# Optimization experiments

Hardware: AMD Instinct MI355X
Metric: run time of the kernel (lower is better)

The kernel has to match this reference:

```python
import jax, jax.numpy as jnp
import numpy as np

B, C, H, W = 8, 256, 64, 64
K = 3                      # kernel size
DG = 4                     # deformable groups
PAD = (K - 1) // 2
K2 = K * K
GN_GROUPS = 32
EPS = 1e-5


def setup_inputs() -> dict:
    key = jax.random.key(0)
    ks = jax.random.split(key, 6)
    x = jax.random.normal(ks[0], (B, C, H, W), dtype=jnp.float32)
    shape = jax.random.normal(ks[1], (B, 4, H, W), dtype=jnp.float32)
    # 1x1 offset conv weight [dg*k*k*2, 4] (bias=False); small std keeps offsets sane
    w_offset = jax.random.normal(ks[2], (DG * K2 * 2, 4), dtype=jnp.float32) * 0.1
    # deformable conv weight [out_c, in_c, K, K]
    w_deform = jax.random.normal(ks[3], (C, C, K, K), dtype=jnp.float32) * 0.01
    gamma = jnp.ones((C,), dtype=jnp.float32)
    beta = jnp.zeros((C,), dtype=jnp.float32)
    return {"x": x, "shape": shape, "w_offset": w_offset,
            "w_deform": w_deform, "gamma": gamma, "beta": beta}


def _bilinear_sample(img, py, px):
    # img: [Cg, H, W]; py, px: [K2, H, W] absolute sampling coords
    h, w = img.shape[1], img.shape[2]
    y0 = jnp.floor(py)
    x0 = jnp.floor(px)
    ly = py - y0
    lx = px - x0

    def gather(yi, xi):
        valid = ((yi >= 0) & (yi <= h - 1) & (xi >= 0) & (xi <= w - 1)).astype(img.dtype)
        yc = jnp.clip(yi, 0, h - 1).astype(jnp.int32)
        xc = jnp.clip(xi, 0, w - 1).astype(jnp.int32)
        return img[:, yc, xc] * valid  # [Cg, K2, H, W]

    v00 = gather(y0, x0)
    v01 = gather(y0, x0 + 1)
    v10 = gather(y0 + 1, x0)
    v11 = gather(y0 + 1, x0 + 1)
    return (v00 * (1 - ly) * (1 - lx) + v01 * (1 - ly) * lx
            + v10 * ly * (1 - lx) + v11 * ly * lx)


def _forward(x, shape, w_offset, w_deform, gamma, beta):
    # offset = 1x1 conv on shape (detached in torch): [B, DG*K2*2, H, W]
    offset = jnp.einsum('oc,bchw->bohw', w_offset, shape)
    # mmcv layout: per group, per kernel position, (dy, dx)
    off = offset.reshape(B, DG, K2, 2, H, W)
    dy, dx = off[:, :, :, 0], off[:, :, :, 1]  # [B, DG, K2, H, W]

    ki = (jnp.arange(K2) // K - PAD).astype(jnp.float32)  # kernel row offsets
    kj = (jnp.arange(K2) % K - PAD).astype(jnp.float32)
    ys = jnp.arange(H, dtype=jnp.float32)
    xs = jnp.arange(W, dtype=jnp.float32)
    # absolute sampling positions [B, DG, K2, H, W]
    py = dy + ki[None, None, :, None, None] + ys[None, None, None, :, None]
    px = dx + kj[None, None, :, None, None] + xs[None, None, None, None, :]

    cg = C // DG
    x_g = x.reshape(B, DG, cg, H, W)
    # sampled: [B, DG, Cg, K2, H, W]
    sampled = jax.vmap(jax.vmap(_bilinear_sample))(x_g, py, px)

    w = w_deform.reshape(C, DG, cg, K2)
    out = jnp.einsum('bgckhw,ogck->bohw', sampled, w)  # [B, C, H, W]

    # GroupNorm(32, C) + ReLU
    og = out.reshape(B, GN_GROUPS, C // GN_GROUPS, H, W)
    mu = og.mean(axis=(2, 3, 4), keepdims=True)
    var = og.var(axis=(2, 3, 4), keepdims=True)
    norm = ((og - mu) * jax.lax.rsqrt(var + EPS)).reshape(B, C, H, W)
    y = norm * gamma[None, :, None, None] + beta[None, :, None, None]
    return jax.nn.relu(y)


def reference(x, shape, w_offset, w_deform, gamma, beta):
    return _forward(x, shape, w_offset, w_deform, gamma, beta)
```

## Files before the change

kernel.cpp:

```cpp
#include <hip/hip_runtime.h>
#include <hip/hip_bf16.h>

#define EPSV 1e-5f

typedef __attribute__((ext_vector_type(8))) short short8;
typedef __attribute__((ext_vector_type(4))) float f32x4;
typedef __attribute__((ext_vector_type(2))) float f32x2;
typedef __attribute__((ext_vector_type(4))) unsigned u32x4;

#define W2_BYTES 1179648ull

__global__ __launch_bounds__(256) void wt2_kernel(const float* __restrict__ wd,
                                                  __hip_bfloat16* __restrict__ w2,
                                                  float* __restrict__ st) {
  int idx = blockIdx.x * 256 + threadIdx.x;
  int c  = idx & 31;
  int r  = idx >> 5;
  int k  = r % 9;
  int r2 = r / 9;
  int p  = r2 & 7;
  int o  = r2 >> 3;
  w2[idx] = __float2bfloat16(wd[(o * 256 + p * 32 + c) * 9 + k]);
  if (blockIdx.x < 2) st[blockIdx.x * 256 + threadIdx.x] = 0.f;
}

static __device__ __forceinline__ f32x2 unpk(unsigned u) {
  union { unsigned i; float f; } lo, hi;
  lo.i = u << 16;
  hi.i = u & 0xffff0000u;
  return (f32x2){lo.f, hi.f};
}

static __device__ __forceinline__ unsigned pkbf(float a, float b) {
  __hip_bfloat162 p = __float22bfloat162_rn(make_float2(a, b));
  return *(unsigned*)&p;
}

__global__ __launch_bounds__(512, 2) void fused_kernel(
    const float* __restrict__ x, const float* __restrict__ shp,
    const float* __restrict__ woff, const __hip_bfloat16* __restrict__ w2,
    float* __restrict__ out, float* __restrict__ st) {
  __shared__ __align__(16) unsigned short sX[2][8 * 64 * 32];
  __shared__ __align__(16) unsigned short sB[2][128 * 32];
  __shared__ float sW[288];

  const int b    = blockIdx.x & 7;
  const int band = blockIdx.x >> 3;
  const int h0   = band << 1;
  const int t    = threadIdx.x;
  const int wv   = t >> 6, lane = t & 63;
  const int quad = lane >> 4, l15 = lane & 15;

  const float* xb = x + ((size_t)b << 20);
  const unsigned short* w2b = (const unsigned short*)w2;

  if (t < 288) sW[t] = woff[t];

  if (wv < 4) {
    const int cw = wv;
    const unsigned short* aro =
        w2b + (size_t)((cw << 6) + l15) * 2304 + (quad << 3);

    f32x4 acc[4][8];
#pragma unroll
    for (int mo = 0; mo < 4; ++mo)
#pragma unroll
      for (int np = 0; np < 8; ++np) acc[mo][np] = (f32x4){0.f, 0.f, 0.f, 0.f};

    short8 afc[4];
#pragma unroll
    for (int mo = 0; mo < 4; ++mo)
      afc[mo] = *(const short8*)(aro + (size_t)(mo << 4) * 2304);

    asm volatile("s_waitcnt lgkmcnt(0)" ::: "memory");
    asm volatile("s_barrier" ::: "memory");
    asm volatile("s_barrier" ::: "memory");

    for (int it = 0; it < 72; ++it) {
      const unsigned short* Bc = sB[it & 1];
#pragma unroll
      for (int np = 0; np < 8; ++np) {
        const int row = (np << 4) + l15;
        short8 bf = *(const short8*)&Bc[(row << 5) + ((quad ^ ((row >> 1) & 3)) << 3)];
#pragma unroll
        for (int mo = 0; mo < 4; ++mo)
          acc[mo][np] = __builtin_amdgcn_mfma_f32_16x16x32_bf16(afc[mo], bf, acc[mo][np], 0, 0, 0);
      }
      if (it < 71) {
#pragma unroll
        for (int mo = 0; mo < 4; ++mo)
          afc[mo] = *(const short8*)(aro + (size_t)(mo << 4) * 2304 + (size_t)((it + 1) << 5));
      }
      asm volatile("s_barrier" ::: "memory");
    }

#pragma unroll
    for (int mo = 0; mo < 4; ++mo) {
      float s = 0.f, q = 0.f;
#pragma unroll
      for (int np = 0; np < 8; ++np)
#pragma unroll
        for (int r = 0; r < 4; ++r) { float v = acc[mo][np][r]; s += v; q += v * v; }
#pragma unroll
      for (int m = 1; m < 16; m <<= 1) { s += __shfl_xor(s, m, 64); q += __shfl_xor(q, m, 64); }
      if (l15 == 0) {
        int gid = (b << 5) + (cw << 3) + (mo << 1) + (quad >> 1);
        atomicAdd(&st[gid], s);
        atomicAdd(&st[256 + gid], q);
      }
    }

    float* ob = out + (((size_t)((b << 8) + (cw << 6))) << 12) + (band << 7);
#pragma unroll
    for (int mo = 0; mo < 4; ++mo)
#pragma unroll
      for (int np = 0; np < 8; ++np)
#pragma unroll
        for (int r = 0; r < 4; ++r)
          ob[((size_t)((mo << 4) + (quad << 2) + r) << 12) + (np << 4) + l15] = acc[mo][np][r];
  } else {
    const int pid   = t - 256;
    const int n     = pid & 127;
    const int chalf = pid >> 7;
    const int pxl   = n & 63;
    const int h     = h0 + (n >> 6);
    const int spx   = pid & 63;
    const int sc8   = (pid >> 6) & 3;
    const int wslot = (sc8 ^ ((spx >> 1) & 3)) << 3;

    float a0 = shp[((size_t)(b * 4 + 0) << 12) + (h << 6) + pxl];
    float a1 = shp[((size_t)(b * 4 + 1) << 12) + (h << 6) + pxl];
    float a2 = shp[((size_t)(b * 4 + 2) << 12) + (h << 6) + pxl];
    float a3 = shp[((size_t)(b * 4 + 3) << 12) + (h << 6) + pxl];

    {
      const float* xph = xb + ((size_t)(sc8 << 3) << 12) + spx;
#pragma unroll
      for (int j = 0; j < 8; ++j) {
        const int grow = min(max(h0 - 3 + j, 0), 63);
        float v[8];
#pragma unroll
        for (int jj = 0; jj < 8; ++jj) v[jj] = xph[(jj << 12) + (grow << 6)];
        *(u32x4*)&sX[0][(((j << 6) + spx) << 5) + wslot] =
            (u32x4){pkbf(v[0], v[1]), pkbf(v[2], v[3]), pkbf(v[4], v[5]), pkbf(v[6], v[7])};
      }
    }

    auto produce = [&](int tp, int tk, int buf) {
      const float* wp = &sW[(((tp >> 1) * 9 + tk)) << 3];
      float dy = wp[0]*a0 + wp[1]*a1 + wp[2]*a2 + wp[3]*a3;
      float dx = wp[4]*a0 + wp[5]*a1 + wp[6]*a2 + wp[7]*a3;
      float py  = dy + (float)(h + tk / 3 - 1);
      float pxp = dx + (float)(pxl + tk % 3 - 1);
      float y0f = floorf(py), x0f = floorf(pxp);
      float ly = py - y0f, lx = pxp - x0f;
      int y0 = (int)y0f, x0 = (int)x0f;
      float m_y0 = (y0 >=  0 && y0 <= 63) ? 1.f : 0.f;
      float m_y1 = (y0 >= -1 && y0 <= 62) ? 1.f : 0.f;
      float m_x0 = (x0 >=  0 && x0 <= 63) ? 1.f : 0.f;
      float m_x1 = (x0 >= -1 && x0 <= 62) ? 1.f : 0.f;
      float w00 = (1.f - ly) * (1.f - lx) * m_y0 * m_x0;
      float w01 = (1.f - ly) * lx         * m_y0 * m_x1;
      float w10 = ly         * (1.f - lx) * m_y1 * m_x0;
      float w11 = ly         * lx         * m_y1 * m_x1;
      int yc0 = min(max(y0, 0), 63),     yc1 = min(max(y0 + 1, 0), 63);
      int xc0 = min(max(x0, 0), 63),     xc1 = min(max(x0 + 1, 0), 63);
      int ry0 = min(max(yc0 - (h0 - 3), 0), 7);
      int ry1 = min(max(yc1 - (h0 - 3), 0), 7);
      const unsigned short* Xc = sX[tp & 1];
      const int s0 = chalf << 1;
      const int z0 = (xc0 >> 1) & 3, z1 = (xc1 >> 1) & 3;
      const int ba = ((ry0 << 6) + xc0) << 5, bb2 = ((ry0 << 6) + xc1) << 5;
      const int bc = ((ry1 << 6) + xc0) << 5, bd = ((ry1 << 6) + xc1) << 5;
      uint4 A0 = *(const uint4*)&Xc[ba  + ((s0 ^ z0) << 3)];
      uint4 A1 = *(const uint4*)&Xc[ba  + (((s0 + 1) ^ z0) << 3)];
      uint4 B0 = *(const uint4*)&Xc[bb2 + ((s0 ^ z1) << 3)];
      uint4 B1 = *(const uint4*)&Xc[bb2 + (((s0 + 1) ^ z1) << 3)];
      uint4 C0 = *(const uint4*)&Xc[bc  + ((s0 ^ z0) << 3)];
      uint4 C1 = *(const uint4*)&Xc[bc  + (((s0 + 1) ^ z0) << 3)];
      uint4 D0 = *(const uint4*)&Xc[bd  + ((s0 ^ z1) << 3)];
      uint4 D1 = *(const uint4*)&Xc[bd  + (((s0 + 1) ^ z1) << 3)];
      unsigned ua[8] = {A0.x, A0.y, A0.z, A0.w, A1.x, A1.y, A1.z, A1.w};
      unsigned ub[8] = {B0.x, B0.y, B0.z, B0.w, B1.x, B1.y, B1.z, B1.w};
      unsigned uc[8] = {C0.x, C0.y, C0.z, C0.w, C1.x, C1.y, C1.z, C1.w};
      unsigned ud[8] = {D0.x, D0.y, D0.z, D0.w, D1.x, D1.y, D1.z, D1.w};
      unsigned ov[8];
#pragma unroll
      for (int j = 0; j < 8; ++j) {
        f32x2 v = unpk(ua[j]) * w00 + unpk(ub[j]) * w01
                + unpk(uc[j]) * w10 + unpk(ud[j]) * w11;
        ov[j] = pkbf(v.x, v.y);
      }
      const int nb5 = n << 5;
      const int zn = (n >> 1) & 3;
      *(u32x4*)&sB[buf][nb5 + ((s0 ^ zn) << 3)]       = (u32x4){ov[0], ov[1], ov[2], ov[3]};
      *(u32x4*)&sB[buf][nb5 + (((s0 + 1) ^ zn) << 3)] = (u32x4){ov[4], ov[5], ov[6], ov[7]};
    };

    auto commit8 = [&](const float* v, int row, int nb) {
      *(u32x4*)&sX[nb][(((row << 6) + spx) << 5) + wslot] =
          (u32x4){pkbf(v[0], v[1]), pkbf(v[2], v[3]), pkbf(v[4], v[5]), pkbf(v[6], v[7])};
    };

    asm volatile("s_waitcnt lgkmcnt(0)" ::: "memory");
    asm volatile("s_barrier" ::: "memory");

    produce(0, 0, 0);
    asm volatile("s_waitcnt lgkmcnt(0)" ::: "memory");
    asm volatile("s_barrier" ::: "memory");

    float xrA[8], xrB[8];
    int k = 0, phase = 0;
    for (int it = 0; it < 72; ++it) {
      if (phase < 7) {
        const float* xph = xb + ((size_t)(((phase + 1) << 5) + (sc8 << 3)) << 12) + spx;
        if (k == 0) {
          const int g0 = min(max(h0 - 3, 0), 63);
          const int g1 = min(max(h0 - 2, 0), 63);
#pragma unroll
          for (int jj = 0; jj < 8; ++jj) xrA[jj] = xph[(jj << 12) + (g0 << 6)];
#pragma unroll
          for (int jj = 0; jj < 8; ++jj) xrB[jj] = xph[(jj << 12) + (g1 << 6)];
        } else if (k <= 7) {
          const int nb = (phase + 1) & 1;
          commit8(xrA, (k == 1) ? 0 : k, nb);
          if (k == 1) commit8(xrB, 1, nb);
          if (k <= 6) {
            const int grow = min(max(h0 - 3 + k + 1, 0), 63);
#pragma unroll
            for (int jj = 0; jj < 8; ++jj) xrA[jj] = xph[(jj << 12) + (grow << 6)];
          }
        }
      }
      if (it < 71) {
        const int tk = (k == 8) ? 0 : k + 1;
        const int tp = (k == 8) ? phase + 1 : phase;
        produce(tp, tk, (it + 1) & 1);
      }
      asm volatile("s_waitcnt lgkmcnt(0)" ::: "memory");
      asm volatile("s_barrier" ::: "memory");
      if (++k == 9) { k = 0; ++phase; }
    }
  }
}

__global__ __launch_bounds__(256) void norm_kernel(float* __restrict__ o,
    const float* __restrict__ st, const float* __restrict__ gamma,
    const float* __restrict__ beta) {
  int idx = blockIdx.x * 256 + threadIdx.x;
  f32x4* p = (f32x4*)o;
  int c = (idx >> 10) & 255;
  int b = idx >> 18;
  int g = b * 32 + (c >> 3);
  const float invn = 1.f / 32768.f;
  float mu  = st[g] * invn;
  float var = st[256 + g] * invn - mu * mu;
  float ga = gamma[c] * rsqrtf(var + EPSV);
  float be = beta[c] - mu * ga;
  f32x4 v = p[idx];
  v.x = fmaxf(fmaf(v.x, ga, be), 0.f);
  v.y = fmaxf(fmaf(v.y, ga, be), 0.f);
  v.z = fmaxf(fmaf(v.z, ga, be), 0.f);
  v.w = fmaxf(fmaf(v.w, ga, be), 0.f);
  __builtin_nontemporal_store(v, &p[idx]);
}

extern "C" void kernel_launch(void* const* d_in, const int* in_sizes, int n_in,
                              void* d_out, int out_size, void* d_ws, size_t ws_size,
                              hipStream_t stream) {
  const float* x     = (const float*)d_in[0];
  const float* shp   = (const float*)d_in[1];
  const float* woff  = (const float*)d_in[2];
  const float* wdef  = (const float*)d_in[3];
  const float* gamma = (const float*)d_in[4];
  const float* beta  = (const float*)d_in[5];
  float* out = (float*)d_out;
  __hip_bfloat16* w2 = (__hip_bfloat16*)d_ws;
  float* st          = (float*)((char*)d_ws + W2_BYTES);

  hipLaunchKernelGGL(wt2_kernel,   dim3(2304), dim3(256), 0, stream, wdef, w2, st);
  hipLaunchKernelGGL(fused_kernel, dim3(256),  dim3(512), 0, stream, x, shp, woff, w2, out, st);
  hipLaunchKernelGGL(norm_kernel,  dim3(8192), dim3(256), 0, stream, out, st, gamma, beta);
}
```

Before: 187.3 us.

## Split fused deformable conv into one-row bands to double block count

Each block now handles a single output row (64 pixels) instead of two, so the grid grows from 256 to 512 blocks and the per-wave accumulator tile halves. The producer warps each sample 8 channels per pixel instead of 16, the B staging buffer shrinks, launch bounds request 4 blocks per CU, and producer waves get raised scheduling priority. The aim is better occupancy and load balance across the CUs. In exchange, each block still stages 8 input rows for only one output row, so input-to-LDS traffic and the weight (A operand) reloads from global double per output.

```diff
diff --git a/kernel.cpp b/kernel.cpp
--- a/kernel.cpp
+++ b/kernel.cpp
@@ -36,17 +36,17 @@
   return *(unsigned*)&p;
 }
 
-__global__ __launch_bounds__(512, 2) void fused_kernel(
+__global__ __launch_bounds__(512, 4) void fused_kernel(
     const float* __restrict__ x, const float* __restrict__ shp,
     const float* __restrict__ woff, const __hip_bfloat16* __restrict__ w2,
     float* __restrict__ out, float* __restrict__ st) {
   __shared__ __align__(16) unsigned short sX[2][8 * 64 * 32];
-  __shared__ __align__(16) unsigned short sB[2][128 * 32];
+  __shared__ __align__(16) unsigned short sB[2][64 * 32];
   __shared__ float sW[288];
 
   const int b    = blockIdx.x & 7;
   const int band = blockIdx.x >> 3;
-  const int h0   = band << 1;
+  const int h    = band;
   const int t    = threadIdx.x;
   const int wv   = t >> 6, lane = t & 63;
   const int quad = lane >> 4, l15 = lane & 15;
@@ -61,11 +61,11 @@
     const unsigned short* aro =
         w2b + (size_t)((cw << 6) + l15) * 2304 + (quad << 3);
 
-    f32x4 acc[4][8];
+    f32x4 acc[4][4];
 #pragma unroll
     for (int mo = 0; mo < 4; ++mo)
 #pragma unroll
-      for (int np = 0; np < 8; ++np) acc[mo][np] = (f32x4){0.f, 0.f, 0.f, 0.f};
+      for (int np = 0; np < 4; ++np) acc[mo][np] = (f32x4){0.f, 0.f, 0.f, 0.f};
 
     short8 afc[4];
 #pragma unroll
@@ -79,7 +79,7 @@
     for (int it = 0; it < 72; ++it) {
       const unsigned short* Bc = sB[it & 1];
 #pragma unroll
-      for (int np = 0; np < 8; ++np) {
+      for (int np = 0; np < 4; ++np) {
         const int row = (np << 4) + l15;
         short8 bf = *(const short8*)&Bc[(row << 5) + ((quad ^ ((row >> 1) & 3)) << 3)];
 #pragma unroll
@@ -98,7 +98,7 @@
     for (int mo = 0; mo < 4; ++mo) {
       float s = 0.f, q = 0.f;
 #pragma unroll
-      for (int np = 0; np < 8; ++np)
+      for (int np = 0; np < 4; ++np)
 #pragma unroll
         for (int r = 0; r < 4; ++r) { float v = acc[mo][np][r]; s += v; q += v * v; }
 #pragma unroll
@@ -110,23 +110,20 @@
       }
     }
 
-    float* ob = out + (((size_t)((b << 8) + (cw << 6))) << 12) + (band << 7);
+    float* ob = out + (((size_t)((b << 8) + (cw << 6))) << 12) + (h << 6);
 #pragma unroll
     for (int mo = 0; mo < 4; ++mo)
 #pragma unroll
-      for (int np = 0; np < 8; ++np)
+      for (int np = 0; np < 4; ++np)
 #pragma unroll
         for (int r = 0; r < 4; ++r)
           ob[((size_t)((mo << 4) + (quad << 2) + r) << 12) + (np << 4) + l15] = acc[mo][np][r];
   } else {
-    const int pid   = t - 256;
-    const int n     = pid & 127;
-    const int chalf = pid >> 7;
-    const int pxl   = n & 63;
-    const int h     = h0 + (n >> 6);
-    const int spx   = pid & 63;
-    const int sc8   = (pid >> 6) & 3;
-    const int wslot = (sc8 ^ ((spx >> 1) & 3)) << 3;
+    __builtin_amdgcn_s_setprio(1);
+    const int pid = t - 256;
+    const int pxl = pid & 63;
+    const int c8  = pid >> 6;
+    const int wslot = (c8 ^ ((pxl >> 1) & 3)) << 3;
 
     float a0 = shp[((size_t)(b * 4 + 0) << 12) + (h << 6) + pxl];
     float a1 = shp[((size_t)(b * 4 + 1) << 12) + (h << 6) + pxl];
@@ -134,14 +131,14 @@
     float a3 = shp[((size_t)(b * 4 + 3) << 12) + (h << 6) + pxl];
 
     {
-      const float* xph = xb + ((size_t)(sc8 << 3) << 12) + spx;
+      const float* xph = xb + ((size_t)(c8 << 3) << 12) + pxl;
 #pragma unroll
       for (int j = 0; j < 8; ++j) {
-        const int grow = min(max(h0 - 3 + j, 0), 63);
+        const int grow = min(max(h - 3 + j, 0), 63);
         float v[8];
 #pragma unroll
         for (int jj = 0; jj < 8; ++jj) v[jj] = xph[(jj << 12) + (grow << 6)];
-        *(u32x4*)&sX[0][(((j << 6) + spx) << 5) + wslot] =
+        *(u32x4*)&sX[0][(((j << 6) + pxl) << 5) + wslot] =
             (u32x4){pkbf(v[0], v[1]), pkbf(v[2], v[3]), pkbf(v[4], v[5]), pkbf(v[6], v[7])};
       }
     }
@@ -165,40 +162,31 @@
       float w11 = ly         * lx         * m_y1 * m_x1;
       int yc0 = min(max(y0, 0), 63),     yc1 = min(max(y0 + 1, 0), 63);
       int xc0 = min(max(x0, 0), 63),     xc1 = min(max(x0 + 1, 0), 63);
-      int ry0 = min(max(yc0 - (h0 - 3), 0), 7);
-      int ry1 = min(max(yc1 - (h0 - 3), 0), 7);
+      int ry0 = min(max(yc0 - (h - 3), 0), 7);
+      int ry1 = min(max(yc1 - (h - 3), 0), 7);
       const unsigned short* Xc = sX[tp & 1];
-      const int s0 = chalf << 1;
       const int z0 = (xc0 >> 1) & 3, z1 = (xc1 >> 1) & 3;
-      const int ba = ((ry0 << 6) + xc0) << 5, bb2 = ((ry0 << 6) + xc1) << 5;
-      const int bc = ((ry1 << 6) + xc0) << 5, bd = ((ry1 << 6) + xc1) << 5;
-      uint4 A0 = *(const uint4*)&Xc[ba  + ((s0 ^ z0) << 3)];
-      uint4 A1 = *(const uint4*)&Xc[ba  + (((s0 + 1) ^ z0) << 3)];
-      uint4 B0 = *(const uint4*)&Xc[bb2 + ((s0 ^ z1) << 3)];
-      uint4 B1 = *(const uint4*)&Xc[bb2 + (((s0 + 1) ^ z1) << 3)];
-      uint4 C0 = *(const uint4*)&Xc[bc  + ((s0 ^ z0) << 3)];
-      uint4 C1 = *(const uint4*)&Xc[bc  + (((s0 + 1) ^ z0) << 3)];
-      uint4 D0 = *(const uint4*)&Xc[bd  + ((s0 ^ z1) << 3)];
-      uint4 D1 = *(const uint4*)&Xc[bd  + (((s0 + 1) ^ z1) << 3)];
-      unsigned ua[8] = {A0.x, A0.y, A0.z, A0.w, A1.x, A1.y, A1.z, A1.w};
-      unsigned ub[8] = {B0.x, B0.y, B0.z, B0.w, B1.x, B1.y, B1.z, B1.w};
-      unsigned uc[8] = {C0.x, C0.y, C0.z, C0.w, C1.x, C1.y, C1.z, C1.w};
-      unsigned ud[8] = {D0.x, D0.y, D0.z, D0.w, D1.x, D1.y, D1.z, D1.w};
-      unsigned ov[8];
-#pragma unroll
-      for (int j = 0; j < 8; ++j) {
+      uint4 Au = *(const uint4*)&Xc[(((ry0 << 6) + xc0) << 5) + ((c8 ^ z0) << 3)];
+      uint4 Bu = *(const uint4*)&Xc[(((ry0 << 6) + xc1) << 5) + ((c8 ^ z1) << 3)];
+      uint4 Cu = *(const uint4*)&Xc[(((ry1 << 6) + xc0) << 5) + ((c8 ^ z0) << 3)];
+      uint4 Du = *(const uint4*)&Xc[(((ry1 << 6) + xc1) << 5) + ((c8 ^ z1) << 3)];
+      unsigned ua[4] = {Au.x, Au.y, Au.z, Au.w};
+      unsigned ub[4] = {Bu.x, Bu.y, Bu.z, Bu.w};
+      unsigned uc[4] = {Cu.x, Cu.y, Cu.z, Cu.w};
+      unsigned ud[4] = {Du.x, Du.y, Du.z, Du.w};
+      unsigned ov[4];
+#pragma unroll
+      for (int j = 0; j < 4; ++j) {
         f32x2 v = unpk(ua[j]) * w00 + unpk(ub[j]) * w01
                 + unpk(uc[j]) * w10 + unpk(ud[j]) * w11;
         ov[j] = pkbf(v.x, v.y);
       }
-      const int nb5 = n << 5;
-      const int zn = (n >> 1) & 3;
-      *(u32x4*)&sB[buf][nb5 + ((s0 ^ zn) << 3)]       = (u32x4){ov[0], ov[1], ov[2], ov[3]};
-      *(u32x4*)&sB[buf][nb5 + (((s0 + 1) ^ zn) << 3)] = (u32x4){ov[4], ov[5], ov[6], ov[7]};
+      *(u32x4*)&sB[buf][(pxl << 5) + ((c8 ^ ((pxl >> 1) & 3)) << 3)] =
+          (u32x4){ov[0], ov[1], ov[2], ov[3]};
     };
 
     auto commit8 = [&](const float* v, int row, int nb) {
-      *(u32x4*)&sX[nb][(((row << 6) + spx) << 5) + wslot] =
+      *(u32x4*)&sX[nb][(((row << 6) + pxl) << 5) + wslot] =
           (u32x4){pkbf(v[0], v[1]), pkbf(v[2], v[3]), pkbf(v[4], v[5]), pkbf(v[6], v[7])};
     };
 
@@ -213,10 +201,10 @@
     int k = 0, phase = 0;
     for (int it = 0; it < 72; ++it) {
       if (phase < 7) {
-        const float* xph = xb + ((size_t)(((phase + 1) << 5) + (sc8 << 3)) << 12) + spx;
+        const float* xph = xb + ((size_t)(((phase + 1) << 5) + (c8 << 3)) << 12) + pxl;
         if (k == 0) {
-          const int g0 = min(max(h0 - 3, 0), 63);
-          const int g1 = min(max(h0 - 2, 0), 63);
+          const int g0 = min(max(h - 3, 0), 63);
+          const int g1 = min(max(h - 2, 0), 63);
 #pragma unroll
           for (int jj = 0; jj < 8; ++jj) xrA[jj] = xph[(jj << 12) + (g0 << 6)];
 #pragma unroll
@@ -226,7 +214,7 @@
           commit8(xrA, (k == 1) ? 0 : k, nb);
           if (k == 1) commit8(xrB, 1, nb);
           if (k <= 6) {
-            const int grow = min(max(h0 - 3 + k + 1, 0), 63);
+            const int grow = min(max(h - 3 + k + 1, 0), 63);
 #pragma unroll
             for (int jj = 0; jj < 8; ++jj) xrA[jj] = xph[(jj << 12) + (grow << 6)];
           }
@@ -279,6 +267,6 @@
   float* st          = (float*)((char*)d_ws + W2_BYTES);
 
   hipLaunchKernelGGL(wt2_kernel,   dim3(2304), dim3(256), 0, stream, wdef, w2, st);
-  hipLaunchKernelGGL(fused_kernel, dim3(256),  dim3(512), 0, stream, x, shp, woff, w2, out, st);
+  hipLaunchKernelGGL(fused_kernel, dim3(512),  dim3(512), 0, stream, x, shp, woff, w2, out, st);
   hipLaunchKernelGGL(norm_kernel,  dim3(8192), dim3(256), 0, stream, out, st, gamma, beta);
 }
```

Measured after the change: 201.1 us. 1.07x slower.

## Double K-step per barrier: producers fill two taps per iteration

Applied to the files above, without the earlier changes.

The producer/consumer loop now runs 36 iterations instead of 72. Each iteration stages two taps, K=64 per pixel, in a wider swizzled sB buffer, so the MMA waves issue twice as many MFMAs between barriers. Each producer thread now handles one tap over all 32 channels rather than half the channels of one tap. The x-tile staging schedule is rewritten to load and commit rows across the new iteration pattern. The aim is to halve barrier and synchronisation overhead, at the cost of more LDS and registers, which may hurt occupancy.

```diff
diff --git a/kernel.cpp b/kernel.cpp
--- a/kernel.cpp
+++ b/kernel.cpp
@@ -41,7 +41,7 @@
     const float* __restrict__ woff, const __hip_bfloat16* __restrict__ w2,
     float* __restrict__ out, float* __restrict__ st) {
   __shared__ __align__(16) unsigned short sX[2][8 * 64 * 32];
-  __shared__ __align__(16) unsigned short sB[2][128 * 32];
+  __shared__ __align__(16) unsigned short sB[2][128 * 64];
   __shared__ float sW[288];
 
   const int b    = blockIdx.x & 7;
@@ -67,29 +67,38 @@
 #pragma unroll
       for (int np = 0; np < 8; ++np) acc[mo][np] = (f32x4){0.f, 0.f, 0.f, 0.f};
 
-    short8 afc[4];
-#pragma unroll
-    for (int mo = 0; mo < 4; ++mo)
-      afc[mo] = *(const short8*)(aro + (size_t)(mo << 4) * 2304);
+    short8 afc[2][4];
+#pragma unroll
+    for (int ks = 0; ks < 2; ++ks)
+#pragma unroll
+      for (int mo = 0; mo < 4; ++mo)
+        afc[ks][mo] = *(const short8*)(aro + (size_t)(mo << 4) * 2304 + (ks << 5));
 
     asm volatile("s_waitcnt lgkmcnt(0)" ::: "memory");
     asm volatile("s_barrier" ::: "memory");
     asm volatile("s_barrier" ::: "memory");
 
-    for (int it = 0; it < 72; ++it) {
+    for (int it = 0; it < 36; ++it) {
       const unsigned short* Bc = sB[it & 1];
 #pragma unroll
       for (int np = 0; np < 8; ++np) {
         const int row = (np << 4) + l15;
-        short8 bf = *(const short8*)&Bc[(row << 5) + ((quad ^ ((row >> 1) & 3)) << 3)];
-#pragma unroll
-        for (int mo = 0; mo < 4; ++mo)
-          acc[mo][np] = __builtin_amdgcn_mfma_f32_16x16x32_bf16(afc[mo], bf, acc[mo][np], 0, 0, 0);
-      }
-      if (it < 71) {
-#pragma unroll
-        for (int mo = 0; mo < 4; ++mo)
-          afc[mo] = *(const short8*)(aro + (size_t)(mo << 4) * 2304 + (size_t)((it + 1) << 5));
+#pragma unroll
+        for (int ks = 0; ks < 2; ++ks) {
+          short8 bf = *(const short8*)&Bc[(row << 6) +
+                         ((((ks << 2) + quad) ^ (row & 7)) << 3)];
+#pragma unroll
+          for (int mo = 0; mo < 4; ++mo)
+            acc[mo][np] = __builtin_amdgcn_mfma_f32_16x16x32_bf16(afc[ks][mo], bf, acc[mo][np], 0, 0, 0);
+        }
+      }
+      if (it < 35) {
+#pragma unroll
+        for (int ks = 0; ks < 2; ++ks)
+#pragma unroll
+          for (int mo = 0; mo < 4; ++mo)
+            afc[ks][mo] = *(const short8*)(aro + (size_t)(mo << 4) * 2304 +
+                                           (size_t)((it + 1) << 6) + (ks << 5));
       }
       asm volatile("s_barrier" ::: "memory");
     }
@@ -119,14 +128,14 @@
         for (int r = 0; r < 4; ++r)
           ob[((size_t)((mo << 4) + (quad << 2) + r) << 12) + (np << 4) + l15] = acc[mo][np][r];
   } else {
-    const int pid   = t - 256;
-    const int n     = pid & 127;
-    const int chalf = pid >> 7;
-    const int pxl   = n & 63;
-    const int h     = h0 + (n >> 6);
-    const int spx   = pid & 63;
-    const int sc8   = (pid >> 6) & 3;
-    const int wslot = (sc8 ^ ((spx >> 1) & 3)) << 3;
+    const int pid     = t - 256;
+    const int pxn     = pid & 127;
+    const int tapslot = pid >> 7;
+    const int pxl     = pxn & 63;
+    const int h       = h0 + (pxn >> 6);
+    const int spx     = pid & 63;
+    const int sc8     = (pid >> 6) & 3;
+    const int wslot   = (sc8 ^ ((spx >> 1) & 3)) << 3;
 
     float a0 = shp[((size_t)(b * 4 + 0) << 12) + (h << 6) + pxl];
     float a1 = shp[((size_t)(b * 4 + 1) << 12) + (h << 6) + pxl];
@@ -141,17 +150,21 @@
         float v[8];
 #pragma unroll
         for (int jj = 0; jj < 8; ++jj) v[jj] = xph[(jj << 12) + (grow << 6)];
-        *(u32x4*)&sX[0][(((j << 6) + spx) << 5) + wslot] =
+        *(u32x4*)&sX[0][((((j << 6) + spx) << 5)) + wslot] =
             (u32x4){pkbf(v[0], v[1]), pkbf(v[2], v[3]), pkbf(v[4], v[5]), pkbf(v[6], v[7])};
       }
     }
 
-    auto produce = [&](int tp, int tk, int buf) {
-      const float* wp = &sW[(((tp >> 1) * 9 + tk)) << 3];
+    auto produce = [&](int g, int buf) {
+      const int ph  = (g * 57) >> 9;
+      const int tap = g - ph * 9;
+      const int kr  = (tap * 11) >> 5;
+      const int kc  = tap - kr * 3;
+      const float* wp = &sW[(((ph >> 1) * 9 + tap)) << 3];
       float dy = wp[0]*a0 + wp[1]*a1 + wp[2]*a2 + wp[3]*a3;
       float dx = wp[4]*a0 + wp[5]*a1 + wp[6]*a2 + wp[7]*a3;
-      float py  = dy + (float)(h + tk / 3 - 1);
-      float pxp = dx + (float)(pxl + tk % 3 - 1);
+      float py  = dy + (float)(h + kr - 1);
+      float pxp = dx + (float)(pxl + kc - 1);
       float y0f = floorf(py), x0f = floorf(pxp);
       float ly = py - y0f, lx = pxp - x0f;
       int y0 = (int)y0f, x0 = (int)x0f;
@@ -167,79 +180,76 @@
       int xc0 = min(max(x0, 0), 63),     xc1 = min(max(x0 + 1, 0), 63);
       int ry0 = min(max(yc0 - (h0 - 3), 0), 7);
       int ry1 = min(max(yc1 - (h0 - 3), 0), 7);
-      const unsigned short* Xc = sX[tp & 1];
-      const int s0 = chalf << 1;
+      const unsigned short* Xc = sX[ph & 1];
       const int z0 = (xc0 >> 1) & 3, z1 = (xc1 >> 1) & 3;
-      const int ba = ((ry0 << 6) + xc0) << 5, bb2 = ((ry0 << 6) + xc1) << 5;
-      const int bc = ((ry1 << 6) + xc0) << 5, bd = ((ry1 << 6) + xc1) << 5;
-      uint4 A0 = *(const uint4*)&Xc[ba  + ((s0 ^ z0) << 3)];
-      uint4 A1 = *(const uint4*)&Xc[ba  + (((s0 + 1) ^ z0) << 3)];
-      uint4 B0 = *(const uint4*)&Xc[bb2 + ((s0 ^ z1) << 3)];
-      uint4 B1 = *(const uint4*)&Xc[bb2 + (((s0 + 1) ^ z1) << 3)];
-      uint4 C0 = *(const uint4*)&Xc[bc  + ((s0 ^ z0) << 3)];
-      uint4 C1 = *(const uint4*)&Xc[bc  + (((s0 + 1) ^ z0) << 3)];
-      uint4 D0 = *(const uint4*)&Xc[bd  + ((s0 ^ z1) << 3)];
-      uint4 D1 = *(const uint4*)&Xc[bd  + (((s0 + 1) ^ z1) << 3)];
-      unsigned ua[8] = {A0.x, A0.y, A0.z, A0.w, A1.x, A1.y, A1.z, A1.w};
-      unsigned ub[8] = {B0.x, B0.y, B0.z, B0.w, B1.x, B1.y, B1.z, B1.w};
-      unsigned uc[8] = {C0.x, C0.y, C0.z, C0.w, C1.x, C1.y, C1.z, C1.w};
-      unsigned ud[8] = {D0.x, D0.y, D0.z, D0.w, D1.x, D1.y, D1.z, D1.w};
-      unsigned ov[8];
-#pragma unroll
-      for (int j = 0; j < 8; ++j) {
-        f32x2 v = unpk(ua[j]) * w00 + unpk(ub[j]) * w01
-                + unpk(uc[j]) * w10 + unpk(ud[j]) * w11;
-        ov[j] = pkbf(v.x, v.y);
-      }
-      const int nb5 = n << 5;
-      const int zn = (n >> 1) & 3;
-      *(u32x4*)&sB[buf][nb5 + ((s0 ^ zn) << 3)]       = (u32x4){ov[0], ov[1], ov[2], ov[3]};
-      *(u32x4*)&sB[buf][nb5 + (((s0 + 1) ^ zn) << 3)] = (u32x4){ov[4], ov[5], ov[6], ov[7]};
+      const int e00 = ((ry0 << 6) + xc0) << 5, e01 = ((ry0 << 6) + xc1) << 5;
+      const int e10 = ((ry1 << 6) + xc0) << 5, e11 = ((ry1 << 6) + xc1) << 5;
+      uint4 Av[4], Bv[4], Cv[4], Dv[4];
+#pragma unroll
+      for (int j = 0; j < 4; ++j) {
+        Av[j] = *(const uint4*)&Xc[e00 + ((j ^ z0) << 3)];
+        Bv[j] = *(const uint4*)&Xc[e01 + ((j ^ z1) << 3)];
+        Cv[j] = *(const uint4*)&Xc[e10 + ((j ^ z0) << 3)];
+        Dv[j] = *(const uint4*)&Xc[e11 + ((j ^ z1) << 3)];
+      }
+#pragma unroll
+      for (int j = 0; j < 4; ++j) {
+        unsigned ua[4] = {Av[j].x, Av[j].y, Av[j].z, Av[j].w};
+        unsigned ub[4] = {Bv[j].x, Bv[j].y, Bv[j].z, Bv[j].w};
+        unsigned uc[4] = {Cv[j].x, Cv[j].y, Cv[j].z, Cv[j].w};
+        unsigned ud[4] = {Dv[j].x, Dv[j].y, Dv[j].z, Dv[j].w};
+        unsigned ov[4];
+#pragma unroll
+        for (int q = 0; q < 4; ++q) {
+          f32x2 v = unpk(ua[q]) * w00 + unpk(ub[q]) * w01
+                  + unpk(uc[q]) * w10 + unpk(ud[q]) * w11;
+          ov[q] = pkbf(v.x, v.y);
+        }
+        *(u32x4*)&sB[buf][(pxn << 6) + ((((tapslot << 2) + j) ^ (pxn & 7)) << 3)] =
+            (u32x4){ov[0], ov[1], ov[2], ov[3]};
+      }
     };
 
-    auto commit8 = [&](const float* v, int row, int nb) {
-      *(u32x4*)&sX[nb][(((row << 6) + spx) << 5) + wslot] =
-          (u32x4){pkbf(v[0], v[1]), pkbf(v[2], v[3]), pkbf(v[4], v[5]), pkbf(v[6], v[7])};
-    };
-
     asm volatile("s_waitcnt lgkmcnt(0)" ::: "memory");
     asm volatile("s_barrier" ::: "memory");
 
-    produce(0, 0, 0);
+    produce(tapslot, 0);
     asm volatile("s_waitcnt lgkmcnt(0)" ::: "memory");
     asm volatile("s_barrier" ::: "memory");
 
-    float xrA[8], xrB[8];
-    int k = 0, phase = 0;
-    for (int it = 0; it < 72; ++it) {
-      if (phase < 7) {
-        const float* xph = xb + ((size_t)(((phase + 1) << 5) + (sc8 << 3)) << 12) + spx;
-        if (k == 0) {
-          const int g0 = min(max(h0 - 3, 0), 63);
-          const int g1 = min(max(h0 - 2, 0), 63);
-#pragma unroll
-          for (int jj = 0; jj < 8; ++jj) xrA[jj] = xph[(jj << 12) + (g0 << 6)];
-#pragma unroll
-          for (int jj = 0; jj < 8; ++jj) xrB[jj] = xph[(jj << 12) + (g1 << 6)];
-        } else if (k <= 7) {
-          const int nb = (phase + 1) & 1;
-          commit8(xrA, (k == 1) ? 0 : k, nb);
-          if (k == 1) commit8(xrB, 1, nb);
-          if (k <= 6) {
-            const int grow = min(max(h0 - 3 + k + 1, 0), 63);
-#pragma unroll
-            for (int jj = 0; jj < 8; ++jj) xrA[jj] = xph[(jj << 12) + (grow << 6)];
+    for (int it = 0; it < 36; ++it) {
+      int s = -1, r0 = 0, nr = 0;
+      if (it <= 2) { s = 1; r0 = it * 3; nr = (it == 2) ? 2 : 3; }
+      else if (it >= 4 && it <= 29) {
+        const int u = it - 4;
+        const int pair = (u * 57) >> 9;
+        const int v = u - pair * 9;
+        if (v < 4)      { s = 2 + (pair << 1); r0 = v << 1; nr = 2; }
+        else if (v < 8) { s = 3 + (pair << 1); r0 = (v - 4) << 1; nr = 2; }
+      }
+      float xr[3][8];
+      if (s > 0) {
+        const float* xph = xb + ((size_t)((s << 5) + (sc8 << 3)) << 12) + spx;
+#pragma unroll
+        for (int rr = 0; rr < 3; ++rr)
+          if (rr < nr) {
+            const int grow = min(max(h0 - 3 + r0 + rr, 0), 63);
+#pragma unroll
+            for (int jj = 0; jj < 8; ++jj) xr[rr][jj] = xph[(jj << 12) + (grow << 6)];
           }
-        }
-      }
-      if (it < 71) {
-        const int tk = (k == 8) ? 0 : k + 1;
-        const int tp = (k == 8) ? phase + 1 : phase;
-        produce(tp, tk, (it + 1) & 1);
+      }
+      if (it < 35) produce(((it + 1) << 1) + tapslot, (it + 1) & 1);
+      if (s > 0) {
+#pragma unroll
+        for (int rr = 0; rr < 3; ++rr)
+          if (rr < nr) {
+            *(u32x4*)&sX[s & 1][((((r0 + rr) << 6) + spx) << 5) + wslot] =
+                (u32x4){pkbf(xr[rr][0], xr[rr][1]), pkbf(xr[rr][2], xr[rr][3]),
+                        pkbf(xr[rr][4], xr[rr][5]), pkbf(xr[rr][6], xr[rr][7])};
+          }
       }
       asm volatile("s_waitcnt lgkmcnt(0)" ::: "memory");
       asm volatile("s_barrier" ::: "memory");
-      if (++k == 9) { k = 0; ++phase; }
     }
   }
 }
```

After: 179.5 us. -4.1%, faster.
